# Optimization experiments

Measured on AMD Instinct MI355X. Metric: run time of the kernel, lower is better.

Reference implementation:

```python
import jax, jax.numpy as jnp
import numpy as np

N = 100000
EPS = 1e-5
NEG_SLOPE = 0.2


def gat_conv(x, src, dst, W, a_src, a_dst, b):
    # x: [N, din]; W: [dout, din]; a_src/a_dst/b: [dout]
    h = x @ W.T                              # [N, dout]
    alpha_s = h @ a_src                      # [N]
    alpha_d = h @ a_dst                      # [N]
    e = jax.nn.leaky_relu(alpha_s[src] + alpha_d[dst], NEG_SLOPE)  # [E]
    # segment softmax over incoming edges of each destination node
    emax = jax.ops.segment_max(e, dst, num_segments=N)
    ex = jnp.exp(e - emax[dst])
    denom = jax.ops.segment_sum(ex, dst, num_segments=N)
    alpha = ex / denom[dst]                  # [E]
    out = jax.ops.segment_sum(alpha[:, None] * h[src], dst, num_segments=N)
    return out + b


def batch_norm(x, gamma, beta):
    mu = jnp.mean(x, axis=0)
    var = jnp.var(x, axis=0)
    return gamma * (x - mu) * jax.lax.rsqrt(var + EPS) + beta


def setup_inputs() -> dict:
    key = jax.random.key(0)
    ks = jax.random.split(key, 20)
    din, dh, dout = 128, 128, 128
    E = 1600000
    x = jax.random.normal(ks[0], (N, din), dtype=jnp.float32)
    edge_index = jax.random.randint(ks[1], (2, E), 0, N, dtype=jnp.int32)
    def glorot(k, shape):
        fan = sum(shape)
        s = jnp.sqrt(6.0 / fan)
        return jax.random.uniform(k, shape, dtype=jnp.float32, minval=-s, maxval=s)
    inp = {"x": x, "edge_index": edge_index}
    dims = [(din, dh), (dh, dh), (dh, dout)]
    for l, (di, do) in enumerate(dims):
        inp[f"W{l}"] = glorot(ks[2 + 4 * l], (do, di))
        inp[f"a_src{l}"] = glorot(ks[3 + 4 * l], (do,)) * 0.1
        inp[f"a_dst{l}"] = glorot(ks[4 + 4 * l], (do,)) * 0.1
        inp[f"b{l}"] = jnp.zeros((do,), dtype=jnp.float32)
    for l in range(2):
        inp[f"gamma{l}"] = jnp.ones((dh,), dtype=jnp.float32)
        inp[f"beta{l}"] = jnp.zeros((dh,), dtype=jnp.float32)
    return inp


def reference(x, edge_index, W0, a_src0, a_dst0, b0, W1, a_src1, a_dst1, b1,
              W2, a_src2, a_dst2, b2, gamma0, beta0, gamma1, beta1):
    # add self-loops (PyG GATConv default)
    ar = jnp.arange(N, dtype=edge_index.dtype)
    src = jnp.concatenate([edge_index[0], ar])
    dst = jnp.concatenate([edge_index[1], ar])
    h = gat_conv(x, src, dst, W0, a_src0, a_dst0, b0)
    h = jax.nn.relu(batch_norm(h, gamma0, beta0))
    h = gat_conv(h, src, dst, W1, a_src1, a_dst1, b1)
    h = jax.nn.relu(batch_norm(h, gamma1, beta1))
    out = gat_conv(h, src, dst, W2, a_src2, a_dst2, b2)
    return out
```

## Files before the change

### kernel.cpp

```cpp
#include <hip/hip_runtime.h>
#include <cstdint>
#include <cstddef>

#define NN 100000
#define NP 100096
#define EE 1600000
#define ET 1700000
#define NBKT 196
#define TILE 2048
#define STAT_BLOCKS 400

typedef short  bf16x8 __attribute__((ext_vector_type(8)));
typedef float  f32x4  __attribute__((ext_vector_type(4)));

__device__ __forceinline__ unsigned short f2bf(float f) {
    unsigned int x = __builtin_bit_cast(unsigned int, f);
    x += 0x7FFFu + ((x >> 16) & 1u);
    return (unsigned short)(x >> 16);
}
__device__ __forceinline__ unsigned int pk2(float lo, float hi) {
    return ((unsigned int)f2bf(hi) << 16) | (unsigned int)f2bf(lo);
}
__device__ __forceinline__ float bflo(unsigned int u) {
    return __builtin_bit_cast(float, u << 16);
}
__device__ __forceinline__ float bfhi(unsigned int u) {
    return __builtin_bit_cast(float, u & 0xFFFF0000u);
}
__device__ __forceinline__ int unperm(int j) { return ((j & 7) << 4) | (j >> 3); }
__device__ __forceinline__ int permf(int c)  { return ((c & 15) << 3) | (c >> 4); }

__global__ void k_pre(const int* __restrict__ ei,
                      const float* __restrict__ W0, const float* __restrict__ W1,
                      const float* __restrict__ W2,
                      const float* __restrict__ as0, const float* __restrict__ ad0,
                      const float* __restrict__ as1, const float* __restrict__ ad1,
                      const float* __restrict__ as2, const float* __restrict__ ad2,
                      unsigned short* __restrict__ Wb, int* __restrict__ btot,
                      float* __restrict__ asv)
{
    const int t = threadIdx.x;
    const int b = blockIdx.x;
    if (b < 256) {
        __shared__ int h[256];
        h[t] = 0;
        __syncthreads();
        for (int e = b * 256 + t; e < ET; e += 256 * 256) {
            int d = (e < EE) ? ei[EE + e] : (e - EE);
            atomicAdd(&h[d >> 9], 1);
        }
        __syncthreads();
        if (h[t]) atomicAdd(&btot[t], h[t]);
    } else if (b < 448) {
        int i = (b - 256) * 256 + t;
        int layer = i >> 14;
        const float* W = (layer == 0) ? W0 : (layer == 1) ? W1 : W2;
        int o  = i & 16383;
        int f  = o >> 3, e = o & 7;
        int nt = f >> 8, k0 = (f >> 6) & 3, lane = f & 63;
        int c  = lane & 15, q = lane >> 4;
        int k  = k0 * 32 + q * 8 + e;
        int col = (layer == 0) ? k : unperm(k);
        Wb[i] = f2bf(W[(nt * 16 + c) * 128 + col]);
    } else {
        const float* Wl[3] = {W0, W1, W2};
        const float* Al[6] = {as0, ad0, as1, ad1, as2, ad2};
        int vec = t >> 7, col = t & 127;
        for (int l = 0; l < 3; ++l) {
            const float* W = Wl[l];
            const float* a = Al[2 * l + vec];
            float s = 0.f;
            for (int n = 0; n < 128; ++n) s += W[n * 128 + col] * a[n];
            int dc = (l == 0) ? col : permf(col);
            asv[l * 256 + vec * 128 + dc] = s;
        }
    }
}

__global__ __launch_bounds__(256) void k_bucket(
    const int* __restrict__ ei, const int* __restrict__ btot,
    int* __restrict__ bcur0, unsigned int* __restrict__ bucketed)
{
    __shared__ int h4[4][256], woff[4][256], loff[256], gbase[256], sc[256], bst[256];
    __shared__ unsigned int stage[TILE];
    __shared__ int gaddr[TILE];
    __shared__ int stot_s;
    const int t = threadIdx.x;
    const int w = t >> 6;
    const int e0 = blockIdx.x * TILE;

    const int v0 = btot[t];
    bst[t] = v0;
    h4[0][t] = 0; h4[1][t] = 0; h4[2][t] = 0; h4[3][t] = 0;
    __syncthreads();
    for (int o = 1; o < 256; o <<= 1) {
        int a = (t >= o) ? bst[t - o] : 0;
        __syncthreads();
        bst[t] += a;
        __syncthreads();
    }
    const int bstart_t = bst[t] - v0;

    unsigned int pk[TILE / 256];
    int bk[TILE / 256];
#pragma unroll
    for (int i = 0; i < TILE / 256; ++i) {
        int e = e0 + i * 256 + t;
        bk[i] = -1;
        if (e < ET) {
            int s, d;
            if (e < EE) { s = ei[e]; d = ei[EE + e]; } else { s = e - EE; d = s; }
            bk[i] = d >> 9;
            pk[i] = ((unsigned int)(d & 511) << 17) | (unsigned int)s;
            atomicAdd(&h4[w][bk[i]], 1);
        }
    }
    __syncthreads();

    int h0 = h4[0][t], h1 = h4[1][t], h2 = h4[2][t], h3 = h4[3][t];
    int tot = h0 + h1 + h2 + h3;
    sc[t] = tot;
    __syncthreads();
    for (int o = 1; o < 256; o <<= 1) {
        int a = (t >= o) ? sc[t - o] : 0;
        __syncthreads();
        sc[t] += a;
        __syncthreads();
    }
    int lo = sc[t] - tot;
    loff[t] = lo;
    woff[0][t] = lo;
    woff[1][t] = lo + h0;
    woff[2][t] = lo + h0 + h1;
    woff[3][t] = lo + h0 + h1 + h2;
    if (t < NBKT && tot) gbase[t] = bstart_t + atomicAdd(&bcur0[t], tot);
    if (t == 255) stot_s = sc[255];
    h4[0][t] = 0; h4[1][t] = 0; h4[2][t] = 0; h4[3][t] = 0;
    __syncthreads();

#pragma unroll
    for (int i = 0; i < TILE / 256; ++i) {
        if (bk[i] >= 0) {
            int b = bk[i];
            int r = woff[w][b] + atomicAdd(&h4[w][b], 1);
            stage[r] = pk[i];
            gaddr[r] = gbase[b] + (r - loff[b]);
        }
    }
    __syncthreads();

    const int stot = stot_s;
    for (int j = t; j < stot; j += 256)
        bucketed[gaddr[j]] = stage[j];
}

__global__ __launch_bounds__(256) void k_csr(
    const unsigned int* __restrict__ bucketed, const int* __restrict__ btot,
    int* __restrict__ off, int* __restrict__ srcs)
{
    __shared__ int h[512], sc2[512], c2[512], sp[256], bst[256];
    __shared__ int s_beg, s_end;
    const int t = threadIdx.x;
    const int b = blockIdx.x;

    const int v0 = btot[t];
    bst[t] = v0;
    __syncthreads();
    for (int o = 1; o < 256; o <<= 1) {
        int a = (t >= o) ? bst[t - o] : 0;
        __syncthreads();
        bst[t] += a;
        __syncthreads();
    }
    if (t == b) { s_end = bst[b]; s_beg = bst[b] - v0; }
    if (b == 0 && t == 0) off[NN] = ET;
    h[t] = 0; h[t + 256] = 0; c2[t] = 0; c2[t + 256] = 0;
    __syncthreads();
    const int beg = s_beg, end = s_end;
    const int cnt = end - beg;

    for (int i = t; i < cnt; i += 256)
        atomicAdd(&h[bucketed[beg + i] >> 17], 1);
    __syncthreads();

    int a0 = h[2 * t], a1 = h[2 * t + 1];
    sp[t] = a0 + a1;
    __syncthreads();
    for (int o = 1; o < 256; o <<= 1) {
        int a = (t >= o) ? sp[t - o] : 0;
        __syncthreads();
        sp[t] += a;
        __syncthreads();
    }
    int ep = sp[t] - (a0 + a1);
    sc2[2 * t] = ep;
    sc2[2 * t + 1] = ep + a0;
    __syncthreads();

    const int d0 = b << 9;
#pragma unroll
    for (int k = t; k < 512; k += 256) {
        int d = d0 + k;
        if (d < NN) off[d] = beg + sc2[k];
    }

    for (int i = t; i < cnt; i += 256) {
        unsigned int v = bucketed[beg + i];
        int ld = v >> 17;
        int r = atomicAdd(&c2[ld], 1);
        srcs[beg + sc2[ld] + r] = (int)(v & 0x1FFFFu);
    }
}

template<int MODE>
__global__ __launch_bounds__(256) void k_mfma(
    const void* __restrict__ Xv, const unsigned short* __restrict__ Wb,
    const float* __restrict__ gsum, const float* __restrict__ gsq,
    const float* __restrict__ gamma, const float* __restrict__ beta,
    const float* __restrict__ wsd,
    unsigned short* __restrict__ Hb, float* __restrict__ AS, float* __restrict__ AD)
{
    __shared__ float ws_s[128], wd_s[128], scale_s[128], shift_s[128];
    const int t    = threadIdx.x;
    const int lane = t & 63;
    const int c    = lane & 15;
    const int q    = lane >> 4;
    const int r0   = blockIdx.x * 64 + (t >> 6) * 16;
    const int row  = r0 + c;

    if (t < 128) {
        ws_s[t] = wsd[t];
        wd_s[t] = wsd[128 + t];
        if (MODE) {
            int ot = unperm(t);
            float mu  = gsum[t] * (1.f / NN);
            float var = gsq[t] * (1.f / NN) - mu * mu;
            float sc  = gamma[ot] * rsqrtf(var + 1e-5f);
            scale_s[t] = sc;
            shift_s[t] = beta[ot] - mu * sc;
        }
    }
    __syncthreads();

    union { uint4 u; bf16x8 v; } Af[4];
    float asp = 0.f, adp = 0.f;
    if (row < NN) {
        if (MODE) {
            const unsigned short* xp = (const unsigned short*)Xv + ((size_t)row << 7) + (q << 3);
#pragma unroll
            for (int k0 = 0; k0 < 4; ++k0) {
                uint4 r = *(const uint4*)(xp + (k0 << 5));
                const int kb = (k0 << 5) + (q << 3);
                float a0 = bflo(r.x), a1 = bfhi(r.x), a2 = bflo(r.y), a3 = bfhi(r.y);
                float a4 = bflo(r.z), a5 = bfhi(r.z), a6 = bflo(r.w), a7 = bfhi(r.w);
                float4 sA = *(const float4*)&scale_s[kb];
                float4 sB = *(const float4*)&scale_s[kb + 4];
                float4 hA = *(const float4*)&shift_s[kb];
                float4 hB = *(const float4*)&shift_s[kb + 4];
                a0 = fmaxf(0.f, fmaf(a0, sA.x, hA.x));
                a1 = fmaxf(0.f, fmaf(a1, sA.y, hA.y));
                a2 = fmaxf(0.f, fmaf(a2, sA.z, hA.z));
                a3 = fmaxf(0.f, fmaf(a3, sA.w, hA.w));
                a4 = fmaxf(0.f, fmaf(a4, sB.x, hB.x));
                a5 = fmaxf(0.f, fmaf(a5, sB.y, hB.y));
                a6 = fmaxf(0.f, fmaf(a6, sB.z, hB.z));
                a7 = fmaxf(0.f, fmaf(a7, sB.w, hB.w));
                float4 wa = *(const float4*)&ws_s[kb];
                float4 wb = *(const float4*)&ws_s[kb + 4];
                float4 da = *(const float4*)&wd_s[kb];
                float4 db = *(const float4*)&wd_s[kb + 4];
                asp = fmaf(a0, wa.x, fmaf(a1, wa.y, fmaf(a2, wa.z, fmaf(a3, wa.w, asp))));
                asp = fmaf(a4, wb.x, fmaf(a5, wb.y, fmaf(a6, wb.z, fmaf(a7, wb.w, asp))));
                adp = fmaf(a0, da.x, fmaf(a1, da.y, fmaf(a2, da.z, fmaf(a3, da.w, adp))));
                adp = fmaf(a4, db.x, fmaf(a5, db.y, fmaf(a6, db.z, fmaf(a7, db.w, adp))));
                Af[k0].u.x = pk2(a0, a1);
                Af[k0].u.y = pk2(a2, a3);
                Af[k0].u.z = pk2(a4, a5);
                Af[k0].u.w = pk2(a6, a7);
            }
        } else {
            const float* xp = (const float*)Xv + ((size_t)row << 7) + (q << 3);
#pragma unroll
            for (int k0 = 0; k0 < 4; ++k0) {
                float4 a = *(const float4*)(xp + (k0 << 5));
                float4 b = *(const float4*)(xp + (k0 << 5) + 4);
                const int kb = (k0 << 5) + (q << 3);
                float4 wa = *(const float4*)&ws_s[kb];
                float4 wb = *(const float4*)&ws_s[kb + 4];
                float4 da = *(const float4*)&wd_s[kb];
                float4 db = *(const float4*)&wd_s[kb + 4];
                asp = fmaf(a.x, wa.x, fmaf(a.y, wa.y, fmaf(a.z, wa.z, fmaf(a.w, wa.w, asp))));
                asp = fmaf(b.x, wb.x, fmaf(b.y, wb.y, fmaf(b.z, wb.z, fmaf(b.w, wb.w, asp))));
                adp = fmaf(a.x, da.x, fmaf(a.y, da.y, fmaf(a.z, da.z, fmaf(a.w, da.w, adp))));
                adp = fmaf(b.x, db.x, fmaf(b.y, db.y, fmaf(b.z, db.z, fmaf(b.w, db.w, adp))));
                Af[k0].u.x = pk2(a.x, a.y);
                Af[k0].u.y = pk2(a.z, a.w);
                Af[k0].u.z = pk2(b.x, b.y);
                Af[k0].u.w = pk2(b.z, b.w);
            }
        }
    } else {
#pragma unroll
        for (int k0 = 0; k0 < 4; ++k0) Af[k0].u = make_uint4(0, 0, 0, 0);
    }

    asp += __shfl_xor(asp, 16); asp += __shfl_xor(asp, 32);
    adp += __shfl_xor(adp, 16); adp += __shfl_xor(adp, 32);
    if (lane < 16) {
        int grow = r0 + lane;
        if (grow < NN) { AS[grow] = asp; AD[grow] = adp; }
    }

    f32x4 acc[8];
#pragma unroll
    for (int nt = 0; nt < 8; ++nt) acc[nt] = (f32x4){0.f, 0.f, 0.f, 0.f};

#pragma unroll
    for (int nt = 0; nt < 8; ++nt) {
        union { uint4 u; bf16x8 v; } Bf[4];
#pragma unroll
        for (int k0 = 0; k0 < 4; ++k0)
            Bf[k0].u = *(const uint4*)(Wb + ((size_t)(((nt << 2) + k0) * 64 + lane) << 3));
#pragma unroll
        for (int k0 = 0; k0 < 4; ++k0)
            acc[nt] = __builtin_amdgcn_mfma_f32_16x16x32_bf16(Af[k0].v, Bf[k0].v, acc[nt], 0, 0, 0);
    }

#pragma unroll
    for (int r = 0; r < 4; ++r) {
        int grow = r0 + q * 4 + r;
        if (grow < NN) {
            uint4 o;
            o.x = pk2(acc[0][r], acc[1][r]);
            o.y = pk2(acc[2][r], acc[3][r]);
            o.z = pk2(acc[4][r], acc[5][r]);
            o.w = pk2(acc[6][r], acc[7][r]);
            *(uint4*)(Hb + ((size_t)grow << 7) + (c << 3)) = o;
        }
    }
}

template<int OUTBF>
__global__ __launch_bounds__(256) void k_agg(
    const int* __restrict__ off, const int* __restrict__ srcs,
    const unsigned short* __restrict__ Hb, const float* __restrict__ AS,
    const float* __restrict__ AD, const float* __restrict__ bias,
    void* __restrict__ OUT)
{
    __shared__ uint2 s_e[4][64];
    const int wid  = threadIdx.x >> 6;
    const int lane = threadIdx.x & 63;
    const int g    = lane >> 4;
    const int x16  = lane & 15;
    const int n    = blockIdx.x * 4 + wid;
    const int beg = off[n], end = off[n + 1];
    const float adn = AD[n];

    float acc[8];
#pragma unroll
    for (int i = 0; i < 8; ++i) acc[i] = 0.f;
    float den = 0.f;

    for (int base = beg; base < end; base += 64) {
        int cnt = end - base; if (cnt > 64) cnt = 64;
        float wgt = 0.f; int s = 0;
        if (lane < cnt) {
            s = srcs[base + lane];
            float e = AS[s] + adn;
            e = (e > 0.f) ? e : 0.2f * e;
            wgt = __expf(e);
        }
        s_e[wid][lane] = make_uint2((unsigned int)s, __builtin_bit_cast(unsigned int, wgt));
        den += wgt;
        int rounds = (cnt + 3) >> 2;
        for (int j = 0; j < rounds; ++j) {
            uint2 ew = s_e[wid][(j << 2) + g];
            float wq = __builtin_bit_cast(float, ew.y);
            uint4 u = *((const uint4*)(Hb + ((size_t)ew.x << 7)) + x16);
            acc[0] = fmaf(wq, bflo(u.x), acc[0]);
            acc[1] = fmaf(wq, bfhi(u.x), acc[1]);
            acc[2] = fmaf(wq, bflo(u.y), acc[2]);
            acc[3] = fmaf(wq, bfhi(u.y), acc[3]);
            acc[4] = fmaf(wq, bflo(u.z), acc[4]);
            acc[5] = fmaf(wq, bfhi(u.z), acc[5]);
            acc[6] = fmaf(wq, bflo(u.w), acc[6]);
            acc[7] = fmaf(wq, bfhi(u.w), acc[7]);
        }
    }

#pragma unroll
    for (int i = 0; i < 8; ++i) {
        acc[i] += __shfl_xor(acc[i], 16);
        acc[i] += __shfl_xor(acc[i], 32);
    }
#pragma unroll
    for (int o = 32; o; o >>= 1) den += __shfl_xor(den, o);
    float inv = 1.f / den;

    if (g == 0) {
        float o8[8];
#pragma unroll
        for (int i = 0; i < 8; ++i)
            o8[i] = fmaf(acc[i], inv, bias[i * 16 + x16]);
        if (OUTBF) {
            uint4 pkd;
            pkd.x = pk2(o8[0], o8[1]); pkd.y = pk2(o8[2], o8[3]);
            pkd.z = pk2(o8[4], o8[5]); pkd.w = pk2(o8[6], o8[7]);
            *(uint4*)((unsigned short*)OUT + ((size_t)n << 7) + (x16 << 3)) = pkd;
        } else {
            float* op = (float*)OUT + ((size_t)n << 7) + x16;
#pragma unroll
            for (int i = 0; i < 8; ++i)
                op[i * 16] = o8[i];
        }
    }
}

__global__ __launch_bounds__(256) void k_colsum(const unsigned int* __restrict__ Xb,
                                                float* __restrict__ gsum, float* __restrict__ gsq) {
    __shared__ float ls[4][128], lq[4][128];
    const int t = threadIdx.x;
    const int c2 = t & 63;
    const int half = t >> 6;
    float s0 = 0.f, s1 = 0.f, q0 = 0.f, q1 = 0.f;
    for (int r = blockIdx.x * 4 + half; r < NN; r += STAT_BLOCKS * 4) {
        unsigned int v = Xb[(size_t)r * 64 + c2];
        float f0 = bflo(v), f1 = bfhi(v);
        s0 += f0; q0 += f0 * f0;
        s1 += f1; q1 += f1 * f1;
    }
    ls[half][2 * c2] = s0; ls[half][2 * c2 + 1] = s1;
    lq[half][2 * c2] = q0; lq[half][2 * c2 + 1] = q1;
    __syncthreads();
    if (t < 128) {
        float ss = ls[0][t] + ls[1][t] + ls[2][t] + ls[3][t];
        float qq = lq[0][t] + lq[1][t] + lq[2][t] + lq[3][t];
        atomicAdd(&gsum[t], ss);
        atomicAdd(&gsq[t], qq);
    }
}

extern "C" void kernel_launch(void* const* d_in, const int* in_sizes, int n_in,
                              void* d_out, int out_size, void* d_ws, size_t ws_size,
                              hipStream_t stream)
{
    const float* x  = (const float*)d_in[0];
    const int*   ei = (const int*)d_in[1];
    const float* Wm[3]  = {(const float*)d_in[2], (const float*)d_in[6],  (const float*)d_in[10]};
    const float* Asr[3] = {(const float*)d_in[3], (const float*)d_in[7],  (const float*)d_in[11]};
    const float* Ads[3] = {(const float*)d_in[4], (const float*)d_in[8],  (const float*)d_in[12]};
    const float* Bs[3]  = {(const float*)d_in[5], (const float*)d_in[9],  (const float*)d_in[13]};
    const float* gam[2] = {(const float*)d_in[14], (const float*)d_in[16]};
    const float* bet[2] = {(const float*)d_in[15], (const float*)d_in[17]};

    char* p = (char*)d_ws;
    auto carve = [&](size_t bytes) -> char* {
        char* r = p;
        p += (bytes + 255) & ~(size_t)255;
        return r;
    };
    int*   off_   = (int*)carve((size_t)(NN + 1) * 4);
    int*   srcs   = (int*)carve((size_t)ET * 4);
    unsigned int* bucketed = (unsigned int*)carve((size_t)ET * 4);
    int*   btot   = (int*)carve(256 * 4);
    int*   bcur0  = (int*)carve(256 * 4);
    float* gstat  = (float*)carve(4 * 128 * 4);
    float* asv    = (float*)carve(3 * 256 * 4);
    unsigned short* Hb  = (unsigned short*)carve((size_t)NP * 128 * 2);
    unsigned short* Wb  = (unsigned short*)carve((size_t)3 * 16384 * 2);
    float* AS    = (float*)carve((size_t)NN * 4);
    float* AD    = (float*)carve((size_t)NN * 4);

    float*          OUTf = (float*)d_out;
    unsigned short* OUTb = (unsigned short*)d_out;

    (void)hipMemsetAsync(btot, 0, 256 * 4 + 256 * 4 + 4 * 128 * 4, stream);

    k_pre<<<449, 256, 0, stream>>>(ei, Wm[0], Wm[1], Wm[2],
                                   Asr[0], Ads[0], Asr[1], Ads[1], Asr[2], Ads[2],
                                   Wb, btot, asv);
    k_bucket<<<(ET + TILE - 1) / TILE, 256, 0, stream>>>(ei, btot, bcur0, bucketed);
    k_csr<<<NBKT, 256, 0, stream>>>(bucketed, btot, off_, srcs);

    const int MFMA_GRID = NP / 64;

    k_mfma<0><<<MFMA_GRID, 256, 0, stream>>>(x, Wb, nullptr, nullptr, nullptr, nullptr,
                                             asv, Hb, AS, AD);
    k_agg<1><<<NN / 4, 256, 0, stream>>>(off_, srcs, Hb, AS, AD, Bs[0], OUTb);
    k_colsum<<<STAT_BLOCKS, 256, 0, stream>>>((const unsigned int*)OUTb, gstat, gstat + 128);

    k_mfma<1><<<MFMA_GRID, 256, 0, stream>>>(OUTb, Wb + 16384, gstat, gstat + 128,
                                             gam[0], bet[0], asv + 256, Hb, AS, AD);
    k_agg<1><<<NN / 4, 256, 0, stream>>>(off_, srcs, Hb, AS, AD, Bs[1], OUTb);
    k_colsum<<<STAT_BLOCKS, 256, 0, stream>>>((const unsigned int*)OUTb, gstat + 256, gstat + 384);

    k_mfma<1><<<MFMA_GRID, 256, 0, stream>>>(OUTb, Wb + 32768, gstat + 256, gstat + 384,
                                             gam[1], bet[1], asv + 512, Hb, AS, AD);
    k_agg<0><<<NN / 4, 256, 0, stream>>>(off_, srcs, Hb, AS, AD, Bs[2], OUTf);
}
```

Baseline: 487.1 us.

## Fuse batch-norm column statistics into aggregation kernel with slotted atomics

Each aggregation kernel that writes a bf16 hidden layer now accumulates per-column sum and sum of squares in registers. It runs as a grid-stride loop over 2500 blocks and flushes its partial sums with atomics into 8 slot copies. The following MFMA kernel adds the slots together when it computes the batch-norm scale and shift. This removes the two separate column-sum kernels and their extra pass over the 100k×128 activations, at the cost of many contended float atomics and statistics taken from unrounded fp32 values. A small unroll pragma is also added to the attention-vector precompute loop.

New measurement: 915.3 us. 1.88x slower.

```diff
diff --git a/kernel.cpp b/kernel.cpp
--- a/kernel.cpp
+++ b/kernel.cpp
@@ -8,7 +8,8 @@
 #define ET 1700000
 #define NBKT 196
 #define TILE 2048
-#define STAT_BLOCKS 400
+#define NSLOT 8
+#define AGG_BLOCKS 2500
 
 typedef short  bf16x8 __attribute__((ext_vector_type(8)));
 typedef float  f32x4  __attribute__((ext_vector_type(4)));
@@ -70,6 +71,7 @@
             const float* W = Wl[l];
             const float* a = Al[2 * l + vec];
             float s = 0.f;
+#pragma unroll 16
             for (int n = 0; n < 128; ++n) s += W[n * 128 + col] * a[n];
             int dc = (l == 0) ? col : permf(col);
             asv[l * 256 + vec * 128 + dc] = s;
@@ -215,7 +217,7 @@
 template<int MODE>
 __global__ __launch_bounds__(256) void k_mfma(
     const void* __restrict__ Xv, const unsigned short* __restrict__ Wb,
-    const float* __restrict__ gsum, const float* __restrict__ gsq,
+    const float* __restrict__ gstat8,
     const float* __restrict__ gamma, const float* __restrict__ beta,
     const float* __restrict__ wsd,
     unsigned short* __restrict__ Hb, float* __restrict__ AS, float* __restrict__ AD)
@@ -232,9 +234,15 @@
         ws_s[t] = wsd[t];
         wd_s[t] = wsd[128 + t];
         if (MODE) {
+            float su = 0.f, sq = 0.f;
+#pragma unroll
+            for (int s = 0; s < NSLOT; ++s) {
+                su += gstat8[s * 256 + t];
+                sq += gstat8[s * 256 + 128 + t];
+            }
             int ot = unperm(t);
-            float mu  = gsum[t] * (1.f / NN);
-            float var = gsq[t] * (1.f / NN) - mu * mu;
+            float mu  = su * (1.f / NN);
+            float var = sq * (1.f / NN) - mu * mu;
             float sc  = gamma[ot] * rsqrtf(var + 1e-5f);
             scale_s[t] = sc;
             shift_s[t] = beta[ot] - mu * sc;
@@ -345,98 +353,97 @@
     const int* __restrict__ off, const int* __restrict__ srcs,
     const unsigned short* __restrict__ Hb, const float* __restrict__ AS,
     const float* __restrict__ AD, const float* __restrict__ bias,
-    void* __restrict__ OUT)
+    void* __restrict__ OUT, float* __restrict__ gstat)
 {
     __shared__ uint2 s_e[4][64];
     const int wid  = threadIdx.x >> 6;
     const int lane = threadIdx.x & 63;
     const int g    = lane >> 4;
     const int x16  = lane & 15;
-    const int n    = blockIdx.x * 4 + wid;
-    const int beg = off[n], end = off[n + 1];
-    const float adn = AD[n];
-
-    float acc[8];
-#pragma unroll
-    for (int i = 0; i < 8; ++i) acc[i] = 0.f;
-    float den = 0.f;
-
-    for (int base = beg; base < end; base += 64) {
-        int cnt = end - base; if (cnt > 64) cnt = 64;
-        float wgt = 0.f; int s = 0;
-        if (lane < cnt) {
-            s = srcs[base + lane];
-            float e = AS[s] + adn;
-            e = (e > 0.f) ? e : 0.2f * e;
-            wgt = __expf(e);
-        }
-        s_e[wid][lane] = make_uint2((unsigned int)s, __builtin_bit_cast(unsigned int, wgt));
-        den += wgt;
-        int rounds = (cnt + 3) >> 2;
-        for (int j = 0; j < rounds; ++j) {
-            uint2 ew = s_e[wid][(j << 2) + g];
-            float wq = __builtin_bit_cast(float, ew.y);
-            uint4 u = *((const uint4*)(Hb + ((size_t)ew.x << 7)) + x16);
-            acc[0] = fmaf(wq, bflo(u.x), acc[0]);
-            acc[1] = fmaf(wq, bfhi(u.x), acc[1]);
-            acc[2] = fmaf(wq, bflo(u.y), acc[2]);
-            acc[3] = fmaf(wq, bfhi(u.y), acc[3]);
-            acc[4] = fmaf(wq, bflo(u.z), acc[4]);
-            acc[5] = fmaf(wq, bfhi(u.z), acc[5]);
-            acc[6] = fmaf(wq, bflo(u.w), acc[6]);
-            acc[7] = fmaf(wq, bfhi(u.w), acc[7]);
-        }
-    }
-
-#pragma unroll
-    for (int i = 0; i < 8; ++i) {
-        acc[i] += __shfl_xor(acc[i], 16);
-        acc[i] += __shfl_xor(acc[i], 32);
-    }
-#pragma unroll
-    for (int o = 32; o; o >>= 1) den += __shfl_xor(den, o);
-    float inv = 1.f / den;
-
-    if (g == 0) {
-        float o8[8];
-#pragma unroll
-        for (int i = 0; i < 8; ++i)
-            o8[i] = fmaf(acc[i], inv, bias[i * 16 + x16]);
-        if (OUTBF) {
-            uint4 pkd;
-            pkd.x = pk2(o8[0], o8[1]); pkd.y = pk2(o8[2], o8[3]);
-            pkd.z = pk2(o8[4], o8[5]); pkd.w = pk2(o8[6], o8[7]);
-            *(uint4*)((unsigned short*)OUT + ((size_t)n << 7) + (x16 << 3)) = pkd;
-        } else {
-            float* op = (float*)OUT + ((size_t)n << 7) + x16;
+    const int stride = gridDim.x * 4;
+
+    float st_s[8], st_q[8];
+    if (OUTBF) {
+#pragma unroll
+        for (int i = 0; i < 8; ++i) { st_s[i] = 0.f; st_q[i] = 0.f; }
+    }
+
+    for (int n = blockIdx.x * 4 + wid; n < NN; n += stride) {
+        const int beg = off[n], end = off[n + 1];
+        const float adn = AD[n];
+
+        float acc[8];
+#pragma unroll
+        for (int i = 0; i < 8; ++i) acc[i] = 0.f;
+        float den = 0.f;
+
+        for (int base = beg; base < end; base += 64) {
+            int cnt = end - base; if (cnt > 64) cnt = 64;
+            float wgt = 0.f; int s = 0;
+            if (lane < cnt) {
+                s = srcs[base + lane];
+                float e = AS[s] + adn;
+                e = (e > 0.f) ? e : 0.2f * e;
+                wgt = __expf(e);
+            }
+            s_e[wid][lane] = make_uint2((unsigned int)s, __builtin_bit_cast(unsigned int, wgt));
+            den += wgt;
+            int rounds = (cnt + 3) >> 2;
+            for (int j = 0; j < rounds; ++j) {
+                uint2 ew = s_e[wid][(j << 2) + g];
+                float wq = __builtin_bit_cast(float, ew.y);
+                uint4 u = *((const uint4*)(Hb + ((size_t)ew.x << 7)) + x16);
+                acc[0] = fmaf(wq, bflo(u.x), acc[0]);
+                acc[1] = fmaf(wq, bfhi(u.x), acc[1]);
+                acc[2] = fmaf(wq, bflo(u.y), acc[2]);
+                acc[3] = fmaf(wq, bfhi(u.y), acc[3]);
+                acc[4] = fmaf(wq, bflo(u.z), acc[4]);
+                acc[5] = fmaf(wq, bfhi(u.z), acc[5]);
+                acc[6] = fmaf(wq, bflo(u.w), acc[6]);
+                acc[7] = fmaf(wq, bfhi(u.w), acc[7]);
+            }
+        }
+
+#pragma unroll
+        for (int i = 0; i < 8; ++i) {
+            acc[i] += __shfl_xor(acc[i], 16);
+            acc[i] += __shfl_xor(acc[i], 32);
+        }
+#pragma unroll
+        for (int o = 32; o; o >>= 1) den += __shfl_xor(den, o);
+        float inv = 1.f / den;
+
+        if (g == 0) {
+            float o8[8];
 #pragma unroll
             for (int i = 0; i < 8; ++i)
-                op[i * 16] = o8[i];
-        }
-    }
-}
-
-__global__ __launch_bounds__(256) void k_colsum(const unsigned int* __restrict__ Xb,
-                                                float* __restrict__ gsum, float* __restrict__ gsq) {
-    __shared__ float ls[4][128], lq[4][128];
-    const int t = threadIdx.x;
-    const int c2 = t & 63;
-    const int half = t >> 6;
-    float s0 = 0.f, s1 = 0.f, q0 = 0.f, q1 = 0.f;
-    for (int r = blockIdx.x * 4 + half; r < NN; r += STAT_BLOCKS * 4) {
-        unsigned int v = Xb[(size_t)r * 64 + c2];
-        float f0 = bflo(v), f1 = bfhi(v);
-        s0 += f0; q0 += f0 * f0;
-        s1 += f1; q1 += f1 * f1;
-    }
-    ls[half][2 * c2] = s0; ls[half][2 * c2 + 1] = s1;
-    lq[half][2 * c2] = q0; lq[half][2 * c2 + 1] = q1;
-    __syncthreads();
-    if (t < 128) {
-        float ss = ls[0][t] + ls[1][t] + ls[2][t] + ls[3][t];
-        float qq = lq[0][t] + lq[1][t] + lq[2][t] + lq[3][t];
-        atomicAdd(&gsum[t], ss);
-        atomicAdd(&gsq[t], qq);
+                o8[i] = fmaf(acc[i], inv, bias[i * 16 + x16]);
+            if (OUTBF) {
+                uint4 pkd;
+                pkd.x = pk2(o8[0], o8[1]); pkd.y = pk2(o8[2], o8[3]);
+                pkd.z = pk2(o8[4], o8[5]); pkd.w = pk2(o8[6], o8[7]);
+                *(uint4*)((unsigned short*)OUT + ((size_t)n << 7) + (x16 << 3)) = pkd;
+#pragma unroll
+                for (int i = 0; i < 8; ++i) {
+                    st_s[i] += o8[i];
+                    st_q[i] = fmaf(o8[i], o8[i], st_q[i]);
+                }
+            } else {
+                float* op = (float*)OUT + ((size_t)n << 7) + x16;
+#pragma unroll
+                for (int i = 0; i < 8; ++i)
+                    op[i * 16] = o8[i];
+            }
+        }
+    }
+
+    if (OUTBF && g == 0) {
+        float* gs = gstat + (blockIdx.x & (NSLOT - 1)) * 256;
+#pragma unroll
+        for (int i = 0; i < 8; ++i) {
+            atomicAdd(&gs[(x16 << 3) + i], st_s[i]);
+            atomicAdd(&gs[128 + (x16 << 3) + i], st_q[i]);
+        }
     }
 }
 
@@ -464,7 +471,7 @@
     unsigned int* bucketed = (unsigned int*)carve((size_t)ET * 4);
     int*   btot   = (int*)carve(256 * 4);
     int*   bcur0  = (int*)carve(256 * 4);
-    float* gstat  = (float*)carve(4 * 128 * 4);
+    float* gstat  = (float*)carve(2 * NSLOT * 256 * 4);
     float* asv    = (float*)carve(3 * 256 * 4);
     unsigned short* Hb  = (unsigned short*)carve((size_t)NP * 128 * 2);
     unsigned short* Wb  = (unsigned short*)carve((size_t)3 * 16384 * 2);
@@ -474,7 +481,7 @@
     float*          OUTf = (float*)d_out;
     unsigned short* OUTb = (unsigned short*)d_out;
 
-    (void)hipMemsetAsync(btot, 0, 256 * 4 + 256 * 4 + 4 * 128 * 4, stream);
+    (void)hipMemsetAsync(btot, 0, 256 * 4 + 256 * 4 + 2 * NSLOT * 256 * 4, stream);
 
     k_pre<<<449, 256, 0, stream>>>(ei, Wm[0], Wm[1], Wm[2],
                                    Asr[0], Ads[0], Asr[1], Ads[1], Asr[2], Ads[2],
@@ -484,17 +491,16 @@
 
     const int MFMA_GRID = NP / 64;
 
-    k_mfma<0><<<MFMA_GRID, 256, 0, stream>>>(x, Wb, nullptr, nullptr, nullptr, nullptr,
+    k_mfma<0><<<MFMA_GRID, 256, 0, stream>>>(x, Wb, nullptr, nullptr, nullptr,
                                              asv, Hb, AS, AD);
-    k_agg<1><<<NN / 4, 256, 0, stream>>>(off_, srcs, Hb, AS, AD, Bs[0], OUTb);
-    k_colsum<<<STAT_BLOCKS, 256, 0, stream>>>((const unsigned int*)OUTb, gstat, gstat + 128);
-
-    k_mfma<1><<<MFMA_GRID, 256, 0, stream>>>(OUTb, Wb + 16384, gstat, gstat + 128,
+    k_agg<1><<<AGG_BLOCKS, 256, 0, stream>>>(off_, srcs, Hb, AS, AD, Bs[0], OUTb, gstat);
+
+    k_mfma<1><<<MFMA_GRID, 256, 0, stream>>>(OUTb, Wb + 16384, gstat,
                                              gam[0], bet[0], asv + 256, Hb, AS, AD);
-    k_agg<1><<<NN / 4, 256, 0, stream>>>(off_, srcs, Hb, AS, AD, Bs[1], OUTb);
-    k_colsum<<<STAT_BLOCKS, 256, 0, stream>>>((const unsigned int*)OUTb, gstat + 256, gstat + 384);
-
-    k_mfma<1><<<MFMA_GRID, 256, 0, stream>>>(OUTb, Wb + 32768, gstat + 256, gstat + 384,
+    k_agg<1><<<AGG_BLOCKS, 256, 0, stream>>>(off_, srcs, Hb, AS, AD, Bs[1], OUTb,
+                                             gstat + NSLOT * 256);
+
+    k_mfma<1><<<MFMA_GRID, 256, 0, stream>>>(OUTb, Wb + 32768, gstat + NSLOT * 256,
                                              gam[1], bet[1], asv + 512, Hb, AS, AD);
-    k_agg<0><<<NN / 4, 256, 0, stream>>>(off_, srcs, Hb, AS, AD, Bs[2], OUTf);
-}
+    k_agg<0><<<NN / 4, 256, 0, stream>>>(off_, srcs, Hb, AS, AD, Bs[2], OUTf, nullptr);
+}
```
